# Kernel tuning notes

Measured on AMD Instinct MI355X. Metric: run time of the kernel, lower is better.

The kernel has to match this reference:

```python
import jax, jax.numpy as jnp
import numpy as np

N = 200_000          # active voxels
CIN, COUT = 64, 128  # in_filters, out_filters
GRID = (32, 480, 480)  # sparse spatial shape (D, H, W)
NEG_SLOPE = 0.01     # nn.LeakyReLU default
EPS = 1e-5           # BatchNorm1d default


def _build_nbrs():
    """Build rulebook-style neighbor tables for the two submanifold kernels.

    Returns nbr31 [9, N] for kernel (3,1,3) and nbr13 [9, N] for kernel (1,3,3).
    Entry == N means 'no active neighbor' (maps to a zero pad row).
    """
    rng = np.random.default_rng(0)
    prod = GRID[0] * GRID[1] * GRID[2]
    lin = rng.choice(prod, size=N, replace=False)
    z, y, x = np.unravel_index(lin, GRID)
    lut = np.full(prod, N, dtype=np.int64)
    lut[lin] = np.arange(N)

    def nbrs(offsets):
        out = np.full((len(offsets), N), N, dtype=np.int32)
        for k, (dz, dy, dx) in enumerate(offsets):
            zz, yy, xx = z + dz, y + dy, x + dx
            valid = ((zz >= 0) & (zz < GRID[0]) & (yy >= 0) & (yy < GRID[1])
                     & (xx >= 0) & (xx < GRID[2]))
            l2 = (zz * GRID[1] + yy) * GRID[2] + xx
            out[k, valid] = lut[l2[valid]].astype(np.int32)
        return out

    off31 = [(dz, 0, dx) for dz in (-1, 0, 1) for dx in (-1, 0, 1)]  # (3,1,3)
    off13 = [(0, dy, dx) for dy in (-1, 0, 1) for dx in (-1, 0, 1)]  # (1,3,3)
    return nbrs(off31), nbrs(off13)


def setup_inputs() -> dict:
    key = jax.random.key(0)
    ks = jax.random.split(key, 5)
    nbr31, nbr13 = _build_nbrs()
    s_in = (2.0 / (9 * CIN)) ** 0.5
    s_out = (2.0 / (9 * COUT)) ** 0.5
    ones = jnp.ones((COUT,), jnp.float32)
    zeros = jnp.zeros((COUT,), jnp.float32)
    return {
        "feats": jax.random.normal(ks[0], (N, CIN), jnp.float32),
        "W1": jax.random.normal(ks[1], (9, CIN, COUT), jnp.float32) * s_in,
        "W1_2": jax.random.normal(ks[2], (9, COUT, COUT), jnp.float32) * s_out,
        "W2": jax.random.normal(ks[3], (9, CIN, COUT), jnp.float32) * s_in,
        "W3": jax.random.normal(ks[4], (9, COUT, COUT), jnp.float32) * s_out,
        "g0": ones, "b0": zeros,      # bn0  (init: weight=1, bias=0)
        "g0_2": ones, "b0_2": zeros,  # bn0_2
        "g1": ones, "b1": zeros,      # bn1
        "g2": ones, "b2": zeros,      # bn2
        "nbr31": jnp.asarray(nbr31),
        "nbr13": jnp.asarray(nbr13),
    }


def _subm_conv(f, W, nbr):
    # f [N, Cin], W [9, Cin, Cout], nbr [9, N] -> [N, Cout]
    fp = jnp.concatenate([f, jnp.zeros((1, f.shape[1]), f.dtype)], axis=0)
    g = fp[nbr]  # gather: [9, N, Cin]
    return jnp.einsum("knc,kcd->nd", g, W)


def _lrelu(f):
    return jnp.where(f >= 0, f, NEG_SLOPE * f)


def _bn(f, gamma, beta):
    # BatchNorm1d training-mode batch stats (biased variance) over voxel dim
    m = jnp.mean(f, axis=0)
    v = jnp.mean(jnp.square(f), axis=0) - m * m
    return (f - m) * jax.lax.rsqrt(v + EPS) * gamma + beta


def reference(feats, W1, W1_2, W2, W3, g0, b0, g0_2, b0_2, g1, b1, g2, b2,
              nbr31, nbr13):
    shortcut = _bn(_lrelu(_subm_conv(feats, W1, nbr31)), g0, b0)
    shortcut = _bn(_lrelu(_subm_conv(shortcut, W1_2, nbr13)), g0_2, b0_2)
    resA = _bn(_lrelu(_subm_conv(feats, W2, nbr13)), g1, b1)
    resA = _bn(_lrelu(_subm_conv(resA, W3, nbr31)), g2, b2)
    return resA + shortcut
```

## Files before the change

### kernel.cpp

```cpp
#include <hip/hip_runtime.h>

#define NV 200000
#define NCH 391
#define PCAP 56
#define CG 3125
#define PN 3516
#define RB1 110

typedef __attribute__((ext_vector_type(8))) short sh8;
typedef __attribute__((ext_vector_type(4))) float f32x4;
typedef __attribute__((ext_vector_type(2))) unsigned int u32x2;

__device__ inline unsigned short f2bf(float f) {
  unsigned int u = __builtin_bit_cast(unsigned int, f);
  u += 0x7FFFu + ((u >> 16) & 1u);
  return (unsigned short)(u >> 16);
}
__device__ inline float bf2f(unsigned short h) {
  unsigned int u = ((unsigned int)h) << 16;
  return __builtin_bit_cast(float, u);
}
__device__ inline float lrelu(float v) { return v >= 0.f ? v : 0.01f * v; }

__global__ __launch_bounds__(256) void prep_k(
    const float* __restrict__ W1, const float* __restrict__ W12,
    const float* __restrict__ W2, const float* __restrict__ W3,
    unsigned short* __restrict__ T1, unsigned short* __restrict__ T12,
    unsigned short* __restrict__ T2, unsigned short* __restrict__ T3,
    const int* __restrict__ nbr31, const int* __restrict__ nbr13,
    int2* __restrict__ pairs, int* __restrict__ cc) {
  __shared__ unsigned short lt[64 * 130];
  __shared__ int base_s[4];
  __shared__ int run;
  int bx = blockIdx.x;
  const int tid = threadIdx.x;
  if (bx < 36) {
    const float* src;
    unsigned short* dst;
    int cin, k;
    if (bx < 9) { src = W1; dst = T1; cin = 64; k = bx; }
    else if (bx < 18) { src = W2; dst = T2; cin = 64; k = bx - 9; }
    else if (bx < 27) { src = W12; dst = T12; cin = 128; k = bx - 18; }
    else { src = W3; dst = T3; cin = 128; k = bx - 27; }
    src += (size_t)k * cin * 128;
    dst += (size_t)k * 128 * cin;
    const int cmask = cin - 1;
    const int csh = (cin == 64) ? 6 : 7;
    for (int h = 0; h < 2; ++h) {
      if (h) __syncthreads();
      const int tot = cin * 64;
      for (int e = tid; e < tot; e += 256) {
        const int c = e >> 6, dd = e & 63;
        lt[dd * 130 + c] = f2bf(src[c * 128 + h * 64 + dd]);
      }
      __syncthreads();
      for (int o = tid; o < tot; o += 256) {
        const int dl = o >> csh, c = o & cmask;
        dst[(size_t)(h * 64 + dl) * cin + c] = lt[dl * 130 + c];
      }
    }
    return;
  }
  bx -= 36;
  const int slot = bx / NCH, chunk = bx % NCH;
  const int table = slot >> 3, kk = slot & 7;
  const int k = kk + (kk >= 4);
  const int* nb = (table ? nbr13 : nbr31) + (size_t)k * NV;
  const int lane = tid & 63, wv = tid >> 6;
  if (tid == 0) run = 0;
  __syncthreads();
  int2* pw = pairs + (size_t)(slot * NCH + chunk) * PCAP;
#pragma unroll
  for (int i = 0; i < 2; ++i) {
    const int n = chunk * 512 + i * 256 + tid;
    const int val = (n < NV) ? nb[n] : NV;
    const bool valid = (val != NV);
    const unsigned long long m = __ballot(valid);
    const int loff = __popcll(m & ((1ull << lane) - 1ull));
    if (lane == 0) base_s[wv] = __popcll(m);
    __syncthreads();
    int wbase = run;
    for (int w = 0; w < wv; ++w) wbase += base_s[w];
    if (valid) {
      const int pos = wbase + loff;
      if (pos < PCAP) {
        int2 pr;
        pr.x = val;
        pr.y = n;
        pw[pos] = pr;
      }
    }
    __syncthreads();
    if (tid == 0) run += base_s[0] + base_s[1] + base_s[2] + base_s[3];
    __syncthreads();
  }
  if (tid == 0) cc[slot * NCH + chunk] = min(run, PCAP);
}

#define STATS_EMIT(ACC, PART)                                                   \
  {                                                                             \
    f32x4 ssum[2], ssq[2];                                                      \
    _Pragma("unroll") for (int mt = 0; mt < 2; ++mt) {                          \
      ssum[mt] = (f32x4){0.f, 0.f, 0.f, 0.f};                                   \
      ssq[mt] = (f32x4){0.f, 0.f, 0.f, 0.f};                                    \
      _Pragma("unroll") for (int nt = 0; nt < 4; ++nt)                          \
          _Pragma("unroll") for (int q = 0; q < 4; ++q) {                       \
        const float f = lrelu(ACC[mt][nt][q]);                                  \
        ssum[mt][q] += f;                                                       \
        ssq[mt][q] += f * f;                                                    \
      }                                                                         \
      _Pragma("unroll") for (int off = 1; off < 16; off <<= 1)                  \
          _Pragma("unroll") for (int q = 0; q < 4; ++q) {                       \
        ssum[mt][q] += __shfl_xor(ssum[mt][q], off);                            \
        ssq[mt][q] += __shfl_xor(ssq[mt][q], off);                              \
      }                                                                         \
      if (l15 == 0) {                                                           \
        const int d0 = (wv * 2 + mt) * 16 + l4 * 4;                             \
        *(f32x4*)(PART + (size_t)blockIdx.x * 256 + d0) = ssum[mt];             \
        *(f32x4*)(PART + (size_t)blockIdx.x * 256 + 128 + d0) = ssq[mt];        \
      }                                                                         \
    }                                                                           \
  }

#define TILE_OUT(ACC, YPTR)                                                     \
  {                                                                             \
    __syncthreads();                                                            \
    _Pragma("unroll") for (int mt = 0; mt < 2; ++mt)                            \
        _Pragma("unroll") for (int nt = 0; nt < 4; ++nt) {                      \
      u32x2 pk;                                                                 \
      pk[0] = (unsigned)f2bf(ACC[mt][nt][0]) |                                  \
              ((unsigned)f2bf(ACC[mt][nt][1]) << 16);                           \
      pk[1] = (unsigned)f2bf(ACC[mt][nt][2]) |                                  \
              ((unsigned)f2bf(ACC[mt][nt][3]) << 16);                           \
      *(u32x2*)(&lds[(nt * 16 + l15) * 136 + (wv * 2 + mt) * 16 + l4 * 4]) = pk;\
    }                                                                           \
    __syncthreads();                                                            \
    _Pragma("unroll") for (int j = 0; j < 4; ++j) {                             \
      const int row = j * 16 + (tid >> 4);                                      \
      const int c16 = tid & 15;                                                 \
      const sh8 v = *(const sh8*)(&lds[row * 136 + c16 * 8]);                   \
      *(sh8*)(YPTR + (size_t)(row0 + row) * 128 + c16 * 8) = v;                 \
    }                                                                           \
  }

__global__ __launch_bounds__(256) void center2_k(
    const float* __restrict__ X, const unsigned short* __restrict__ W1t,
    const unsigned short* __restrict__ W2t, unsigned short* __restrict__ Y1,
    unsigned short* __restrict__ Y2, float* __restrict__ PA,
    float* __restrict__ PB) {
  constexpr int CIN = 64, CH = 8;
  __shared__ unsigned short lds[64 * 136];
  const int tid = threadIdx.x, lane = tid & 63, wv = tid >> 6;
  const int l15 = lane & 15, l4 = lane >> 4;
  const int row0 = blockIdx.x * 64;
  const int js = tid & 7;
#pragma unroll
  for (int i = 0; i < 2; ++i) {
    const int r = (i * 256 + tid) >> 3;
    const f32x4 a = *(const f32x4*)(X + (size_t)(row0 + r) * CIN + js * 8);
    const f32x4 b = *(const f32x4*)(X + (size_t)(row0 + r) * CIN + js * 8 + 4);
    sh8 o;
#pragma unroll
    for (int j = 0; j < 4; ++j) {
      o[j] = (short)f2bf(a[j]);
      o[4 + j] = (short)f2bf(b[j]);
    }
    *(sh8*)(lds + ((size_t)r * CH + (js ^ (r & 7))) * 8) = o;
  }
  __syncthreads();

  f32x4 acc1[2][4], acc2[2][4];
#pragma unroll
  for (int mt = 0; mt < 2; ++mt)
#pragma unroll
    for (int nt = 0; nt < 4; ++nt) {
      acc1[mt][nt] = (f32x4){0.f, 0.f, 0.f, 0.f};
      acc2[mt][nt] = (f32x4){0.f, 0.f, 0.f, 0.f};
    }
  const unsigned short* W1K = W1t + (size_t)(4 * 128) * CIN;
  const unsigned short* W2K = W2t + (size_t)(4 * 128) * CIN;
#pragma unroll
  for (int s = 0; s < 2; ++s) {
    sh8 aw1[2], aw2[2];
#pragma unroll
    for (int mt = 0; mt < 2; ++mt) {
      const int d = (wv * 2 + mt) * 16 + l15;
      aw1[mt] = *(const sh8*)(W1K + (size_t)d * CIN + s * 32 + l4 * 8);
      aw2[mt] = *(const sh8*)(W2K + (size_t)d * CIN + s * 32 + l4 * 8);
    }
#pragma unroll
    for (int nt = 0; nt < 4; ++nt) {
      const int r = nt * 16 + l15;
      const int j = s * 4 + l4;
      const sh8 bx = *(const sh8*)(lds + ((size_t)r * CH + (j ^ (r & 7))) * 8);
#pragma unroll
      for (int mt = 0; mt < 2; ++mt) {
        acc1[mt][nt] =
            __builtin_amdgcn_mfma_f32_16x16x32_bf16(aw1[mt], bx, acc1[mt][nt], 0, 0, 0);
        acc2[mt][nt] =
            __builtin_amdgcn_mfma_f32_16x16x32_bf16(aw2[mt], bx, acc2[mt][nt], 0, 0, 0);
      }
    }
  }
  STATS_EMIT(acc1, PA)
  STATS_EMIT(acc2, PB)
  TILE_OUT(acc1, Y1)
  __syncthreads();
  TILE_OUT(acc2, Y2)
}

__global__ __launch_bounds__(256) void c128_k(
    const unsigned short* __restrict__ X, const unsigned short* __restrict__ Wt,
    const float* __restrict__ abp, unsigned short* __restrict__ Y,
    float* __restrict__ PART) {
  constexpr int CIN = 128, CH = 16;
  __shared__ unsigned short lds[64 * 136];
  const int row0 = blockIdx.x * 64;
  const int tid = threadIdx.x, lane = tid & 63, wv = tid >> 6;
  const int l15 = lane & 15, l4 = lane >> 4;
  const int js = tid & 15;
  const f32x4 aL = *(const f32x4*)(abp + js * 8);
  const f32x4 aH = *(const f32x4*)(abp + js * 8 + 4);
  const f32x4 bL = *(const f32x4*)(abp + 128 + js * 8);
  const f32x4 bH = *(const f32x4*)(abp + 128 + js * 8 + 4);
#pragma unroll
  for (int i = 0; i < 4; ++i) {
    const int r = (i * 256 + tid) >> 4;
    const sh8 v = *(const sh8*)(X + (size_t)(row0 + r) * CIN + js * 8);
    sh8 o;
#pragma unroll
    for (int j = 0; j < 4; ++j) {
      o[j] = (short)f2bf(lrelu(bf2f((unsigned short)v[j])) * aL[j] + bL[j]);
      o[4 + j] = (short)f2bf(lrelu(bf2f((unsigned short)v[4 + j])) * aH[j] + bH[j]);
    }
    *(sh8*)(lds + ((size_t)r * CH + (js ^ (r & 7))) * 8) = o;
  }
  __syncthreads();

  f32x4 acc[2][4];
#pragma unroll
  for (int mt = 0; mt < 2; ++mt)
#pragma unroll
    for (int nt = 0; nt < 4; ++nt) acc[mt][nt] = (f32x4){0.f, 0.f, 0.f, 0.f};

  const unsigned short* WtK = Wt + (size_t)(4 * 128) * CIN;
#pragma unroll
  for (int s = 0; s < 4; ++s) {
    sh8 aw[2];
#pragma unroll
    for (int mt = 0; mt < 2; ++mt) {
      const int d = (wv * 2 + mt) * 16 + l15;
      aw[mt] = *(const sh8*)(WtK + (size_t)d * CIN + s * 32 + l4 * 8);
    }
#pragma unroll
    for (int nt = 0; nt < 4; ++nt) {
      const int r = nt * 16 + l15;
      const int j = s * 4 + l4;
      const sh8 bxv = *(const sh8*)(lds + ((size_t)r * CH + (j ^ (r & 7))) * 8);
#pragma unroll
      for (int mt = 0; mt < 2; ++mt)
        acc[mt][nt] =
            __builtin_amdgcn_mfma_f32_16x16x32_bf16(aw[mt], bxv, acc[mt][nt], 0, 0, 0);
    }
  }
  STATS_EMIT(acc, PART)
  TILE_OUT(acc, Y)
}

__global__ __launch_bounds__(256) void off64_k(
    const float* __restrict__ X, const unsigned short* __restrict__ T1,
    const unsigned short* __restrict__ T2, const int2* __restrict__ pairs,
    const int* __restrict__ cc, unsigned short* __restrict__ y1,
    unsigned short* __restrict__ y2, float* __restrict__ PA,
    float* __restrict__ PB) {
  constexpr int CIN = 64, CH = 8;
  const int layer = blockIdx.x / NCH, chunk = blockIdx.x % NCH;
  const unsigned short* Wt = layer ? T2 : T1;
  unsigned short* Y = layer ? y2 : y1;
  float* PD = layer ? PB : PA;
  const int* ccl = cc + layer * 8 * NCH;
  const int2* pl = pairs + (size_t)layer * 8 * NCH * PCAP;
  __shared__ unsigned short tile[64 * CIN];
  __shared__ int sin[64], sout[64];
  const int tid = threadIdx.x, lane = tid & 63, wv = tid >> 6;
  const int l15 = lane & 15, l4 = lane >> 4;
  const int js = tid & 7;
  f32x4 ds[2], dq[2];
#pragma unroll
  for (int mt = 0; mt < 2; ++mt) {
    ds[mt] = (f32x4){0.f, 0.f, 0.f, 0.f};
    dq[mt] = (f32x4){0.f, 0.f, 0.f, 0.f};
  }

  for (int kk = 0; kk < 8; ++kk) {
    const int n0 = ccl[kk * NCH + chunk];
    if (n0 == 0) continue;
    const int k = kk + (kk >= 4);
    const unsigned short* WtK = Wt + (size_t)k * 128 * CIN;
    __syncthreads();
    if (tid < 64) {
      int2 pr;
      if (tid < n0) pr = pl[(size_t)(kk * NCH + chunk) * PCAP + tid];
      else { pr.x = NV; pr.y = NV; }
      sin[tid] = pr.x;
      sout[tid] = pr.y;
    }
    __syncthreads();
#pragma unroll
    for (int i = 0; i < 2; ++i) {
      const int r = (i * 256 + tid) >> 3;
      const int in = sin[r];
      sh8 o = (sh8){0, 0, 0, 0, 0, 0, 0, 0};
      if (in != NV) {
        const f32x4 a = *(const f32x4*)(X + (size_t)in * CIN + js * 8);
        const f32x4 b = *(const f32x4*)(X + (size_t)in * CIN + js * 8 + 4);
#pragma unroll
        for (int j = 0; j < 4; ++j) {
          o[j] = (short)f2bf(a[j]);
          o[4 + j] = (short)f2bf(b[j]);
        }
      }
      *(sh8*)(tile + ((size_t)r * CH + (js ^ (r & 7))) * 8) = o;
    }
    __syncthreads();

    f32x4 acc[2][4];
#pragma unroll
    for (int mt = 0; mt < 2; ++mt)
#pragma unroll
      for (int nt = 0; nt < 4; ++nt) acc[mt][nt] = (f32x4){0.f, 0.f, 0.f, 0.f};
#pragma unroll
    for (int s = 0; s < 2; ++s) {
      sh8 aw[2];
#pragma unroll
      for (int mt = 0; mt < 2; ++mt) {
        const int d = (wv * 2 + mt) * 16 + l15;
        aw[mt] = *(const sh8*)(WtK + (size_t)d * CIN + s * 32 + l4 * 8);
      }
#pragma unroll
      for (int nt = 0; nt < 4; ++nt) {
        const int r = nt * 16 + l15;
        const int j = s * 4 + l4;
        const sh8 bxv = *(const sh8*)(tile + ((size_t)r * CH + (j ^ (r & 7))) * 8);
#pragma unroll
        for (int mt = 0; mt < 2; ++mt)
          acc[mt][nt] =
              __builtin_amdgcn_mfma_f32_16x16x32_bf16(aw[mt], bxv, acc[mt][nt], 0, 0, 0);
      }
    }
#pragma unroll
    for (int mt = 0; mt < 2; ++mt)
#pragma unroll
      for (int nt = 0; nt < 4; ++nt) {
        const int out = sout[nt * 16 + l15];
        if (out == NV) continue;
        const int d0 = (wv * 2 + mt) * 16 + l4 * 4;
        unsigned short* p = Y + (size_t)out * 128 + d0;
        const u32x2 old = *(const u32x2*)p;
        u32x2 nw;
        float of[4], sf[4];
        of[0] = bf2f((unsigned short)(old[0] & 0xffff));
        of[1] = bf2f((unsigned short)(old[0] >> 16));
        of[2] = bf2f((unsigned short)(old[1] & 0xffff));
        of[3] = bf2f((unsigned short)(old[1] >> 16));
#pragma unroll
        for (int q = 0; q < 4; ++q) {
          sf[q] = of[q] + acc[mt][nt][q];
          const float ln = lrelu(sf[q]), lo = lrelu(of[q]);
          ds[mt][q] += ln - lo;
          dq[mt][q] += ln * ln - lo * lo;
        }
        nw[0] = (unsigned)f2bf(sf[0]) | ((unsigned)f2bf(sf[1]) << 16);
        nw[1] = (unsigned)f2bf(sf[2]) | ((unsigned)f2bf(sf[3]) << 16);
        *(u32x2*)p = nw;
      }
  }
#pragma unroll
  for (int mt = 0; mt < 2; ++mt) {
#pragma unroll
    for (int off = 1; off < 16; off <<= 1)
#pragma unroll
      for (int q = 0; q < 4; ++q) {
        ds[mt][q] += __shfl_xor(ds[mt][q], off);
        dq[mt][q] += __shfl_xor(dq[mt][q], off);
      }
    if (l15 == 0) {
      const int d0 = (wv * 2 + mt) * 16 + l4 * 4;
      *(f32x4*)(PD + (size_t)(CG + chunk) * 256 + d0) = ds[mt];
      *(f32x4*)(PD + (size_t)(CG + chunk) * 256 + 128 + d0) = dq[mt];
    }
  }
}

__global__ __launch_bounds__(256) void off128_k(
    const unsigned short* __restrict__ X, const unsigned short* __restrict__ Wt,
    const int2* __restrict__ pairs_t, const int* __restrict__ cc_t,
    const float* __restrict__ abp, unsigned short* __restrict__ Y,
    float* __restrict__ PD) {
  constexpr int CIN = 128, CH = 16;
  const int chunk = blockIdx.x;
  __shared__ unsigned short tile[64 * CIN];
  __shared__ int sin[64], sout[64];
  const int tid = threadIdx.x, lane = tid & 63, wv = tid >> 6;
  const int l15 = lane & 15, l4 = lane >> 4;
  const int js = tid & 15;
  const f32x4 aL = *(const f32x4*)(abp + js * 8);
  const f32x4 aH = *(const f32x4*)(abp + js * 8 + 4);
  const f32x4 bL = *(const f32x4*)(abp + 128 + js * 8);
  const f32x4 bH = *(const f32x4*)(abp + 128 + js * 8 + 4);
  f32x4 ds[2], dq[2];
#pragma unroll
  for (int mt = 0; mt < 2; ++mt) {
    ds[mt] = (f32x4){0.f, 0.f, 0.f, 0.f};
    dq[mt] = (f32x4){0.f, 0.f, 0.f, 0.f};
  }

  for (int kk = 0; kk < 8; ++kk) {
    const int n0 = cc_t[kk * NCH + chunk];
    if (n0 == 0) continue;
    const int k = kk + (kk >= 4);
    const unsigned short* WtK = Wt + (size_t)k * 128 * CIN;
    __syncthreads();
    if (tid < 64) {
      int2 pr;
      if (tid < n0) pr = pairs_t[(size_t)(kk * NCH + chunk) * PCAP + tid];
      else { pr.x = NV; pr.y = NV; }
      sin[tid] = pr.x;
      sout[tid] = pr.y;
    }
    __syncthreads();
#pragma unroll
    for (int i = 0; i < 4; ++i) {
      const int r = (i * 256 + tid) >> 4;
      const int in = sin[r];
      sh8 o = (sh8){0, 0, 0, 0, 0, 0, 0, 0};
      if (in != NV) {
        const sh8 v = *(const sh8*)(X + (size_t)in * CIN + js * 8);
#pragma unroll
        for (int j = 0; j < 4; ++j) {
          o[j] = (short)f2bf(lrelu(bf2f((unsigned short)v[j])) * aL[j] + bL[j]);
          o[4 + j] = (short)f2bf(lrelu(bf2f((unsigned short)v[4 + j])) * aH[j] + bH[j]);
        }
      }
      *(sh8*)(tile + ((size_t)r * CH + (js ^ (r & 7))) * 8) = o;
    }
    __syncthreads();

    f32x4 acc[2][4];
#pragma unroll
    for (int mt = 0; mt < 2; ++mt)
#pragma unroll
      for (int nt = 0; nt < 4; ++nt) acc[mt][nt] = (f32x4){0.f, 0.f, 0.f, 0.f};
#pragma unroll
    for (int s = 0; s < 4; ++s) {
      sh8 aw[2];
#pragma unroll
      for (int mt = 0; mt < 2; ++mt) {
        const int d = (wv * 2 + mt) * 16 + l15;
        aw[mt] = *(const sh8*)(WtK + (size_t)d * CIN + s * 32 + l4 * 8);
      }
#pragma unroll
      for (int nt = 0; nt < 4; ++nt) {
        const int r = nt * 16 + l15;
        const int j = s * 4 + l4;
        const sh8 bxv = *(const sh8*)(tile + ((size_t)r * CH + (j ^ (r & 7))) * 8);
#pragma unroll
        for (int mt = 0; mt < 2; ++mt)
          acc[mt][nt] =
              __builtin_amdgcn_mfma_f32_16x16x32_bf16(aw[mt], bxv, acc[mt][nt], 0, 0, 0);
      }
    }
#pragma unroll
    for (int mt = 0; mt < 2; ++mt)
#pragma unroll
      for (int nt = 0; nt < 4; ++nt) {
        const int out = sout[nt * 16 + l15];
        if (out == NV) continue;
        const int d0 = (wv * 2 + mt) * 16 + l4 * 4;
        unsigned short* p = Y + (size_t)out * 128 + d0;
        const u32x2 old = *(const u32x2*)p;
        u32x2 nw;
        float of[4], sf[4];
        of[0] = bf2f((unsigned short)(old[0] & 0xffff));
        of[1] = bf2f((unsigned short)(old[0] >> 16));
        of[2] = bf2f((unsigned short)(old[1] & 0xffff));
        of[3] = bf2f((unsigned short)(old[1] >> 16));
#pragma unroll
        for (int q = 0; q < 4; ++q) {
          sf[q] = of[q] + acc[mt][nt][q];
          const float ln = lrelu(sf[q]), lo = lrelu(of[q]);
          ds[mt][q] += ln - lo;
          dq[mt][q] += ln * ln - lo * lo;
        }
        nw[0] = (unsigned)f2bf(sf[0]) | ((unsigned)f2bf(sf[1]) << 16);
        nw[1] = (unsigned)f2bf(sf[2]) | ((unsigned)f2bf(sf[3]) << 16);
        *(u32x2*)p = nw;
      }
  }
#pragma unroll
  for (int mt = 0; mt < 2; ++mt) {
#pragma unroll
    for (int off = 1; off < 16; off <<= 1)
#pragma unroll
      for (int q = 0; q < 4; ++q) {
        ds[mt][q] += __shfl_xor(ds[mt][q], off);
        dq[mt][q] += __shfl_xor(dq[mt][q], off);
      }
    if (l15 == 0) {
      const int d0 = (wv * 2 + mt) * 16 + l4 * 4;
      *(f32x4*)(PD + (size_t)(CG + chunk) * 256 + d0) = ds[mt];
      *(f32x4*)(PD + (size_t)(CG + chunk) * 256 + 128 + d0) = dq[mt];
    }
  }
}

__global__ __launch_bounds__(256) void red1_k(const float* __restrict__ PA,
                                              const float* __restrict__ PB,
                                              float* __restrict__ RA,
                                              float* __restrict__ RB) {
  const int tb = blockIdx.x / RB1;
  const int b = blockIdx.x % RB1;
  const float* P = tb ? PB : PA;
  float* R = tb ? RB : RA;
  const int c = threadIdx.x;
  const int r0 = b * 32;
  const int r1 = (r0 + 32 < PN) ? r0 + 32 : PN;
  float s = 0.f;
#pragma unroll 4
  for (int r = r0; r < r1; ++r) s += P[(size_t)r * 256 + c];
  R[(size_t)b * 256 + c] = s;
}

__global__ __launch_bounds__(1024) void fin2_k(
    const float* __restrict__ RA, const float* __restrict__ gA,
    const float* __restrict__ btA, float* __restrict__ abA,
    const float* __restrict__ RB, const float* __restrict__ gB,
    const float* __restrict__ btB, float* __restrict__ abB) {
  const float* R = blockIdx.x ? RB : RA;
  const float* g = blockIdx.x ? gB : gA;
  const float* bt = blockIdx.x ? btB : btA;
  float* abo = blockIdx.x ? abB : abA;
  __shared__ float S[1024];
  const int t = threadIdx.x;
  const int c = t & 255, grp = t >> 8;
  float s = 0.f;
  for (int b = grp; b < RB1; b += 4) s += R[(size_t)b * 256 + c];
  S[t] = s;
  __syncthreads();
  if (t < 256) S[t] = S[t] + S[256 + t] + S[512 + t] + S[768 + t];
  __syncthreads();
  if (t < 128) {
    const float m = S[t] * (1.0f / (float)NV);
    const float v = S[128 + t] * (1.0f / (float)NV) - m * m;
    const float a = g[t] * rsqrtf(v + 1e-5f);
    abo[t] = a;
    abo[128 + t] = bt[t] - m * a;
  }
}

__global__ __launch_bounds__(256) void final_k(const unsigned short* __restrict__ y3,
                                               const unsigned short* __restrict__ ysc,
                                               const float* __restrict__ ab3,
                                               const float* __restrict__ ab1,
                                               float* __restrict__ out) {
  const long i = (long)blockIdx.x * 256 + threadIdx.x;
  if (i >= (long)NV * 16) return;
  const long base = i * 8;
  const int c0 = (int)(base & 127);
  const sh8 v3 = *(const sh8*)(y3 + base);
  const sh8 vs = *(const sh8*)(ysc + base);
  const f32x4 a3L = *(const f32x4*)(ab3 + c0);
  const f32x4 a3H = *(const f32x4*)(ab3 + c0 + 4);
  const f32x4 b3L = *(const f32x4*)(ab3 + 128 + c0);
  const f32x4 b3H = *(const f32x4*)(ab3 + 128 + c0 + 4);
  const f32x4 a1L = *(const f32x4*)(ab1 + c0);
  const f32x4 a1H = *(const f32x4*)(ab1 + c0 + 4);
  const f32x4 b1L = *(const f32x4*)(ab1 + 128 + c0);
  const f32x4 b1H = *(const f32x4*)(ab1 + 128 + c0 + 4);
  f32x4 oL, oH;
#pragma unroll
  for (int j = 0; j < 4; ++j) {
    oL[j] = a3L[j] * lrelu(bf2f((unsigned short)v3[j])) + b3L[j] +
            a1L[j] * lrelu(bf2f((unsigned short)vs[j])) + b1L[j];
    oH[j] = a3H[j] * lrelu(bf2f((unsigned short)v3[4 + j])) + b3H[j] +
            a1H[j] * lrelu(bf2f((unsigned short)vs[4 + j])) + b1H[j];
  }
  *(f32x4*)(out + base) = oL;
  *(f32x4*)(out + base + 4) = oH;
}

extern "C" void kernel_launch(void* const* d_in, const int* in_sizes, int n_in,
                              void* d_out, int out_size, void* d_ws, size_t ws_size,
                              hipStream_t stream) {
  const float* feats = (const float*)d_in[0];
  const float* W1 = (const float*)d_in[1];
  const float* W12 = (const float*)d_in[2];
  const float* W2 = (const float*)d_in[3];
  const float* W3 = (const float*)d_in[4];
  const float* g0 = (const float*)d_in[5];
  const float* b0 = (const float*)d_in[6];
  const float* g02 = (const float*)d_in[7];
  const float* b02 = (const float*)d_in[8];
  const float* g1 = (const float*)d_in[9];
  const float* b1 = (const float*)d_in[10];
  const float* g2 = (const float*)d_in[11];
  const float* b2 = (const float*)d_in[12];
  const int* nbr31 = (const int*)d_in[13];
  const int* nbr13 = (const int*)d_in[14];
  float* out = (float*)d_out;

  char* ws = (char*)d_ws;
  size_t off = 0;
  auto alloc = [&](size_t bytes) {
    char* p = ws + off;
    off = (off + bytes + 255) & ~(size_t)255;
    return p;
  };

  unsigned short* T1 = (unsigned short*)alloc((size_t)9 * 128 * 64 * 2);
  unsigned short* T2 = (unsigned short*)alloc((size_t)9 * 128 * 64 * 2);
  unsigned short* T12 = (unsigned short*)alloc((size_t)9 * 128 * 128 * 2);
  unsigned short* T3 = (unsigned short*)alloc((size_t)9 * 128 * 128 * 2);
  unsigned short* y1 = (unsigned short*)alloc((size_t)NV * 128 * 2);
  unsigned short* ysc = (unsigned short*)alloc((size_t)NV * 128 * 2);
  unsigned short* y2 = (unsigned short*)alloc((size_t)NV * 128 * 2);
  float* PA = (float*)alloc((size_t)PN * 256 * 4);
  float* PB = (float*)alloc((size_t)PN * 256 * 4);
  float* RA = (float*)alloc((size_t)RB1 * 256 * 4);
  float* RB = (float*)alloc((size_t)RB1 * 256 * 4);
  float* ab = (float*)alloc(1024 * 4);
  int* cc = (int*)alloc((size_t)16 * NCH * 4);
  int2* pairs = (int2*)alloc((size_t)16 * NCH * PCAP * 8);
  unsigned short* y3 = y1;

  const int2* pairs31 = pairs;
  const int2* pairs13 = pairs + (size_t)8 * NCH * PCAP;
  const int* cc31 = cc;
  const int* cc13 = cc + 8 * NCH;


  prep_k<<<36 + 16 * NCH, 256, 0, stream>>>(W1, W12, W2, W3, T1, T12, T2, T3,
                                            nbr31, nbr13, pairs, cc);
  center2_k<<<CG, 256, 0, stream>>>(feats, T1, T2, y1, y2, PA, PB);
  off64_k<<<2 * NCH, 256, 0, stream>>>(feats, T1, T2, pairs, cc, y1, y2, PA, PB);
  red1_k<<<2 * RB1, 256, 0, stream>>>(PA, PB, RA, RB);
  fin2_k<<<2, 1024, 0, stream>>>(RA, g0, b0, ab + 0, RB, g1, b1, ab + 256);
  c128_k<<<CG, 256, 0, stream>>>(y1, T12, ab + 0, ysc, PA);
  off128_k<<<NCH, 256, 0, stream>>>(y1, T12, pairs13, cc13, ab + 0, ysc, PA);
  c128_k<<<CG, 256, 0, stream>>>(y2, T3, ab + 256, y3, PB);
  off128_k<<<NCH, 256, 0, stream>>>(y2, T3, pairs31, cc31, ab + 256, y3, PB);
  red1_k<<<2 * RB1, 256, 0, stream>>>(PA, PB, RA, RB);
  fin2_k<<<2, 1024, 0, stream>>>(RA, g02, b02, ab + 512, RB, g2, b2, ab + 768);
  final_k<<<12500, 256, 0, stream>>>(y3, ysc, ab + 768, ab + 512, out);
}
```

Measured before the change: 282.0 us.

## Merge second-layer conv launches and halve neighbor chunk size for more blocks

New measurement: 306.3 us. 1.09x slower.

```diff
diff --git a/kernel.cpp b/kernel.cpp
--- a/kernel.cpp
+++ b/kernel.cpp
@@ -1,11 +1,11 @@
 #include <hip/hip_runtime.h>
 
 #define NV 200000
-#define NCH 391
-#define PCAP 56
+#define NCH 782
+#define PCAP 32
 #define CG 3125
-#define PN 3516
-#define RB1 110
+#define PN 3907
+#define RB1 123
 
 typedef __attribute__((ext_vector_type(8))) short sh8;
 typedef __attribute__((ext_vector_type(4))) float f32x4;
@@ -31,7 +31,6 @@
     int2* __restrict__ pairs, int* __restrict__ cc) {
   __shared__ unsigned short lt[64 * 130];
   __shared__ int base_s[4];
-  __shared__ int run;
   int bx = blockIdx.x;
   const int tid = threadIdx.x;
   if (bx < 36) {
@@ -67,37 +66,32 @@
   const int k = kk + (kk >= 4);
   const int* nb = (table ? nbr13 : nbr31) + (size_t)k * NV;
   const int lane = tid & 63, wv = tid >> 6;
-  if (tid == 0) run = 0;
+  const int n = chunk * 256 + tid;
+  const int val = (n < NV) ? nb[n] : NV;
+  const bool valid = (val != NV);
+  const unsigned long long m = __ballot(valid);
+  const int loff = __popcll(m & ((1ull << lane) - 1ull));
+  if (lane == 0) base_s[wv] = __popcll(m);
   __syncthreads();
+  int wbase = 0;
+  for (int w = 0; w < wv; ++w) wbase += base_s[w];
   int2* pw = pairs + (size_t)(slot * NCH + chunk) * PCAP;
-#pragma unroll
-  for (int i = 0; i < 2; ++i) {
-    const int n = chunk * 512 + i * 256 + tid;
-    const int val = (n < NV) ? nb[n] : NV;
-    const bool valid = (val != NV);
-    const unsigned long long m = __ballot(valid);
-    const int loff = __popcll(m & ((1ull << lane) - 1ull));
-    if (lane == 0) base_s[wv] = __popcll(m);
-    __syncthreads();
-    int wbase = run;
-    for (int w = 0; w < wv; ++w) wbase += base_s[w];
-    if (valid) {
-      const int pos = wbase + loff;
-      if (pos < PCAP) {
-        int2 pr;
-        pr.x = val;
-        pr.y = n;
-        pw[pos] = pr;
-      }
-    }
-    __syncthreads();
-    if (tid == 0) run += base_s[0] + base_s[1] + base_s[2] + base_s[3];
-    __syncthreads();
-  }
-  if (tid == 0) cc[slot * NCH + chunk] = min(run, PCAP);
-}
-
-#define STATS_EMIT(ACC, PART)                                                   \
+  if (valid) {
+    const int pos = wbase + loff;
+    if (pos < PCAP) {
+      int2 pr;
+      pr.x = val;
+      pr.y = n;
+      pw[pos] = pr;
+    }
+  }
+  if (tid == 0) {
+    const int tot = base_s[0] + base_s[1] + base_s[2] + base_s[3];
+    cc[slot * NCH + chunk] = min(tot, PCAP);
+  }
+}
+
+#define STATS_EMIT(ACC, PART, PROW)                                             \
   {                                                                             \
     f32x4 ssum[2], ssq[2];                                                      \
     _Pragma("unroll") for (int mt = 0; mt < 2; ++mt) {                          \
@@ -116,8 +110,8 @@
       }                                                                         \
       if (l15 == 0) {                                                           \
         const int d0 = (wv * 2 + mt) * 16 + l4 * 4;                             \
-        *(f32x4*)(PART + (size_t)blockIdx.x * 256 + d0) = ssum[mt];             \
-        *(f32x4*)(PART + (size_t)blockIdx.x * 256 + 128 + d0) = ssq[mt];        \
+        *(f32x4*)(PART + (size_t)(PROW)*256 + d0) = ssum[mt];                   \
+        *(f32x4*)(PART + (size_t)(PROW)*256 + 128 + d0) = ssq[mt];              \
       }                                                                         \
     }                                                                           \
   }
@@ -152,7 +146,8 @@
   __shared__ unsigned short lds[64 * 136];
   const int tid = threadIdx.x, lane = tid & 63, wv = tid >> 6;
   const int l15 = lane & 15, l4 = lane >> 4;
-  const int row0 = blockIdx.x * 64;
+  const int prow = blockIdx.x;
+  const int row0 = prow * 64;
   const int js = tid & 7;
 #pragma unroll
   for (int i = 0; i < 2; ++i) {
@@ -202,20 +197,30 @@
       }
     }
   }
-  STATS_EMIT(acc1, PA)
-  STATS_EMIT(acc2, PB)
+  STATS_EMIT(acc1, PA, prow)
+  STATS_EMIT(acc2, PB, prow)
   TILE_OUT(acc1, Y1)
   __syncthreads();
   TILE_OUT(acc2, Y2)
 }
 
-__global__ __launch_bounds__(256) void c128_k(
-    const unsigned short* __restrict__ X, const unsigned short* __restrict__ Wt,
-    const float* __restrict__ abp, unsigned short* __restrict__ Y,
-    float* __restrict__ PART) {
+__global__ __launch_bounds__(256) void c128m_k(
+    const unsigned short* __restrict__ y1, const unsigned short* __restrict__ y2,
+    const unsigned short* __restrict__ T12, const unsigned short* __restrict__ T3,
+    const float* __restrict__ ab, unsigned short* __restrict__ ysc,
+    unsigned short* __restrict__ y3, float* __restrict__ PA,
+    float* __restrict__ PB) {
   constexpr int CIN = 128, CH = 16;
   __shared__ unsigned short lds[64 * 136];
-  const int row0 = blockIdx.x * 64;
+  const int bx = blockIdx.x;
+  const bool first = bx < CG;
+  const unsigned short* X = first ? y1 : y2;
+  const unsigned short* Wt = first ? T12 : T3;
+  const float* abp = first ? ab : ab + 256;
+  unsigned short* Y = first ? ysc : y3;
+  float* PART = first ? PA : PB;
+  const int prow = first ? bx : bx - CG;
+  const int row0 = prow * 64;
   const int tid = threadIdx.x, lane = tid & 63, wv = tid >> 6;
   const int l15 = lane & 15, l4 = lane >> 4;
   const int js = tid & 15;
@@ -263,7 +268,7 @@
             __builtin_amdgcn_mfma_f32_16x16x32_bf16(aw[mt], bxv, acc[mt][nt], 0, 0, 0);
     }
   }
-  STATS_EMIT(acc, PART)
+  STATS_EMIT(acc, PART, prow)
   TILE_OUT(acc, Y)
 }
 
@@ -280,11 +285,12 @@
   float* PD = layer ? PB : PA;
   const int* ccl = cc + layer * 8 * NCH;
   const int2* pl = pairs + (size_t)layer * 8 * NCH * PCAP;
-  __shared__ unsigned short tile[64 * CIN];
-  __shared__ int sin[64], sout[64];
+  __shared__ unsigned short tile[32 * CIN];
+  __shared__ int sin[32], sout[32];
   const int tid = threadIdx.x, lane = tid & 63, wv = tid >> 6;
   const int l15 = lane & 15, l4 = lane >> 4;
   const int js = tid & 7;
+  const int sr = tid >> 3;
   f32x4 ds[2], dq[2];
 #pragma unroll
   for (int mt = 0; mt < 2; ++mt) {
@@ -298,7 +304,7 @@
     const int k = kk + (kk >= 4);
     const unsigned short* WtK = Wt + (size_t)k * 128 * CIN;
     __syncthreads();
-    if (tid < 64) {
+    if (tid < 32) {
       int2 pr;
       if (tid < n0) pr = pl[(size_t)(kk * NCH + chunk) * PCAP + tid];
       else { pr.x = NV; pr.y = NV; }
@@ -306,10 +312,8 @@
       sout[tid] = pr.y;
     }
     __syncthreads();
-#pragma unroll
-    for (int i = 0; i < 2; ++i) {
-      const int r = (i * 256 + tid) >> 3;
-      const int in = sin[r];
+    {
+      const int in = sin[sr];
       sh8 o = (sh8){0, 0, 0, 0, 0, 0, 0, 0};
       if (in != NV) {
         const f32x4 a = *(const f32x4*)(X + (size_t)in * CIN + js * 8);
@@ -320,15 +324,15 @@
           o[4 + j] = (short)f2bf(b[j]);
         }
       }
-      *(sh8*)(tile + ((size_t)r * CH + (js ^ (r & 7))) * 8) = o;
+      *(sh8*)(tile + ((size_t)sr * CH + (js ^ (sr & 7))) * 8) = o;
     }
     __syncthreads();
 
-    f32x4 acc[2][4];
+    f32x4 acc[2][2];
 #pragma unroll
     for (int mt = 0; mt < 2; ++mt)
 #pragma unroll
-      for (int nt = 0; nt < 4; ++nt) acc[mt][nt] = (f32x4){0.f, 0.f, 0.f, 0.f};
+      for (int nt = 0; nt < 2; ++nt) acc[mt][nt] = (f32x4){0.f, 0.f, 0.f, 0.f};
 #pragma unroll
     for (int s = 0; s < 2; ++s) {
       sh8 aw[2];
@@ -338,7 +342,7 @@
         aw[mt] = *(const sh8*)(WtK + (size_t)d * CIN + s * 32 + l4 * 8);
       }
 #pragma unroll
-      for (int nt = 0; nt < 4; ++nt) {
+      for (int nt = 0; nt < 2; ++nt) {
         const int r = nt * 16 + l15;
         const int j = s * 4 + l4;
         const sh8 bxv = *(const sh8*)(tile + ((size_t)r * CH + (j ^ (r & 7))) * 8);
@@ -351,7 +355,7 @@
 #pragma unroll
     for (int mt = 0; mt < 2; ++mt)
 #pragma unroll
-      for (int nt = 0; nt < 4; ++nt) {
+      for (int nt = 0; nt < 2; ++nt) {
         const int out = sout[nt * 16 + l15];
         if (out == NV) continue;
         const int d0 = (wv * 2 + mt) * 16 + l4 * 4;
@@ -392,15 +396,24 @@
   }
 }
 
-__global__ __launch_bounds__(256) void off128_k(
-    const unsigned short* __restrict__ X, const unsigned short* __restrict__ Wt,
-    const int2* __restrict__ pairs_t, const int* __restrict__ cc_t,
-    const float* __restrict__ abp, unsigned short* __restrict__ Y,
-    float* __restrict__ PD) {
+__global__ __launch_bounds__(256) void off128m_k(
+    const unsigned short* __restrict__ y1, const unsigned short* __restrict__ y2,
+    const unsigned short* __restrict__ T12, const unsigned short* __restrict__ T3,
+    const int2* __restrict__ pairs, const int* __restrict__ cc,
+    const float* __restrict__ ab, unsigned short* __restrict__ ysc,
+    unsigned short* __restrict__ y3, float* __restrict__ PA,
+    float* __restrict__ PB) {
   constexpr int CIN = 128, CH = 16;
-  const int chunk = blockIdx.x;
-  __shared__ unsigned short tile[64 * CIN];
-  __shared__ int sin[64], sout[64];
+  const int lay = blockIdx.x / NCH, chunk = blockIdx.x % NCH;
+  const unsigned short* X = lay ? y2 : y1;
+  const unsigned short* Wt = lay ? T3 : T12;
+  const float* abp = lay ? ab + 256 : ab;
+  unsigned short* Y = lay ? y3 : ysc;
+  float* PD = lay ? PB : PA;
+  const int2* pt = pairs + (lay ? 0 : (size_t)8 * NCH * PCAP);
+  const int* ct = cc + (lay ? 0 : 8 * NCH);
+  __shared__ unsigned short tile[32 * CIN];
+  __shared__ int sin[32], sout[32];
   const int tid = threadIdx.x, lane = tid & 63, wv = tid >> 6;
   const int l15 = lane & 15, l4 = lane >> 4;
   const int js = tid & 15;
@@ -416,21 +429,21 @@
   }
 
   for (int kk = 0; kk < 8; ++kk) {
-    const int n0 = cc_t[kk * NCH + chunk];
+    const int n0 = ct[kk * NCH + chunk];
     if (n0 == 0) continue;
     const int k = kk + (kk >= 4);
     const unsigned short* WtK = Wt + (size_t)k * 128 * CIN;
     __syncthreads();
-    if (tid < 64) {
+    if (tid < 32) {
       int2 pr;
-      if (tid < n0) pr = pairs_t[(size_t)(kk * NCH + chunk) * PCAP + tid];
+      if (tid < n0) pr = pt[(size_t)(kk * NCH + chunk) * PCAP + tid];
       else { pr.x = NV; pr.y = NV; }
       sin[tid] = pr.x;
       sout[tid] = pr.y;
     }
     __syncthreads();
 #pragma unroll
-    for (int i = 0; i < 4; ++i) {
+    for (int i = 0; i < 2; ++i) {
       const int r = (i * 256 + tid) >> 4;
       const int in = sin[r];
       sh8 o = (sh8){0, 0, 0, 0, 0, 0, 0, 0};
@@ -446,11 +459,11 @@
     }
     __syncthreads();
 
-    f32x4 acc[2][4];
+    f32x4 acc[2][2];
 #pragma unroll
     for (int mt = 0; mt < 2; ++mt)
 #pragma unroll
-      for (int nt = 0; nt < 4; ++nt) acc[mt][nt] = (f32x4){0.f, 0.f, 0.f, 0.f};
+      for (int nt = 0; nt < 2; ++nt) acc[mt][nt] = (f32x4){0.f, 0.f, 0.f, 0.f};
 #pragma unroll
     for (int s = 0; s < 4; ++s) {
       sh8 aw[2];
@@ -460,7 +473,7 @@
         aw[mt] = *(const sh8*)(WtK + (size_t)d * CIN + s * 32 + l4 * 8);
       }
 #pragma unroll
-      for (int nt = 0; nt < 4; ++nt) {
+      for (int nt = 0; nt < 2; ++nt) {
         const int r = nt * 16 + l15;
         const int j = s * 4 + l4;
         const sh8 bxv = *(const sh8*)(tile + ((size_t)r * CH + (j ^ (r & 7))) * 8);
@@ -473,7 +486,7 @@
 #pragma unroll
     for (int mt = 0; mt < 2; ++mt)
 #pragma unroll
-      for (int nt = 0; nt < 4; ++nt) {
+      for (int nt = 0; nt < 2; ++nt) {
         const int out = sout[nt * 16 + l15];
         if (out == NV) continue;
         const int d0 = (wv * 2 + mt) * 16 + l4 * 4;
@@ -622,8 +635,9 @@
   unsigned short* T12 = (unsigned short*)alloc((size_t)9 * 128 * 128 * 2);
   unsigned short* T3 = (unsigned short*)alloc((size_t)9 * 128 * 128 * 2);
   unsigned short* y1 = (unsigned short*)alloc((size_t)NV * 128 * 2);
+  unsigned short* y2 = (unsigned short*)alloc((size_t)NV * 128 * 2);
   unsigned short* ysc = (unsigned short*)alloc((size_t)NV * 128 * 2);
-  unsigned short* y2 = (unsigned short*)alloc((size_t)NV * 128 * 2);
+  unsigned short* y3 = (unsigned short*)alloc((size_t)NV * 128 * 2);
   float* PA = (float*)alloc((size_t)PN * 256 * 4);
   float* PB = (float*)alloc((size_t)PN * 256 * 4);
   float* RA = (float*)alloc((size_t)RB1 * 256 * 4);
@@ -631,12 +645,6 @@
   float* ab = (float*)alloc(1024 * 4);
   int* cc = (int*)alloc((size_t)16 * NCH * 4);
   int2* pairs = (int2*)alloc((size_t)16 * NCH * PCAP * 8);
-  unsigned short* y3 = y1;
-
-  const int2* pairs31 = pairs;
-  const int2* pairs13 = pairs + (size_t)8 * NCH * PCAP;
-  const int* cc31 = cc;
-  const int* cc13 = cc + 8 * NCH;
 
 
   prep_k<<<36 + 16 * NCH, 256, 0, stream>>>(W1, W12, W2, W3, T1, T12, T2, T3,
@@ -645,10 +653,9 @@
   off64_k<<<2 * NCH, 256, 0, stream>>>(feats, T1, T2, pairs, cc, y1, y2, PA, PB);
   red1_k<<<2 * RB1, 256, 0, stream>>>(PA, PB, RA, RB);
   fin2_k<<<2, 1024, 0, stream>>>(RA, g0, b0, ab + 0, RB, g1, b1, ab + 256);
-  c128_k<<<CG, 256, 0, stream>>>(y1, T12, ab + 0, ysc, PA);
-  off128_k<<<NCH, 256, 0, stream>>>(y1, T12, pairs13, cc13, ab + 0, ysc, PA);
-  c128_k<<<CG, 256, 0, stream>>>(y2, T3, ab + 256, y3, PB);
-  off128_k<<<NCH, 256, 0, stream>>>(y2, T3, pairs31, cc31, ab + 256, y3, PB);
+  c128m_k<<<2 * CG, 256, 0, stream>>>(y1, y2, T12, T3, ab, ysc, y3, PA, PB);
+  off128m_k<<<2 * NCH, 256, 0, stream>>>(y1, y2, T12, T3, pairs, cc, ab, ysc, y3,
+                                         PA, PB);
   red1_k<<<2 * RB1, 256, 0, stream>>>(PA, PB, RA, RB);
   fin2_k<<<2, 1024, 0, stream>>>(RA, g02, b02, ab + 512, RB, g2, b2, ab + 768);
   final_k<<<12500, 256, 0, stream>>>(y3, ysc, ab + 768, ab + 512, out);
```
